# Kernel tuning notes

Measured on AMD Instinct MI355X. Metric: run time of the kernel, lower is better.

## Reference

```python
import jax, jax.numpy as jnp
import numpy as np


def _ln(x, w, b, eps=1e-5):
    m = x.mean(-1, keepdims=True)
    v = jnp.mean((x - m) ** 2, -1, keepdims=True)
    return (x - m) / jnp.sqrt(v + eps) * w + b


def _conv_layer(x, batch, pos, mask, Ncount, wq, bq, wk, bk, wv, bv):
    # x: [N, C] node features; dense-batched to [B, L, C] per to_dense_batch
    B, L = mask.shape
    C = x.shape[-1]
    H = wq.shape[1] // C  # out_channels == hidden == C
    D = C
    xd = jnp.zeros((B, L, C), x.dtype).at[batch, pos].set(x)
    qs = (xd @ wq + bq).reshape(B, L, H, D)
    ks = (xd @ wk + bk).reshape(B, L, H, D)
    vs = (xd @ wv + bv).reshape(B, L, H, D)
    m = mask[:, :, None, None]
    qs = jnp.where(m, qs, 0.0)
    ks = jnp.where(m, ks, 0.0)
    vs = jnp.where(m, vs, 0.0)
    # NOTE: original divides by GLOBAL Frobenius norm of the whole tensor
    qs = qs / jnp.linalg.norm(qs)
    ks = ks / jnp.linalg.norm(ks)
    Nb = Ncount[:, None, None, None]  # [B,1,1,1] node count per graph
    kvs = jnp.einsum('blhm,blhd->bhmd', ks, vs)
    num = jnp.einsum('bnhm,bhmd->bnhd', qs, kvs) + Nb * vs
    ks_sum = ks.sum(1)  # [B,H,D]
    denom = jnp.einsum('bnhm,bhm->bnh', qs, ks_sum)[..., None] + Nb
    out = num / denom  # [B,L,H,D]
    return out[batch, pos].mean(1)  # gather masked rows, mean over heads -> [N, D]


def _forward(x, fc0_w, fc0_b, ln0_w, ln0_b,
             wq0_w, wq0_b, wk0_w, wk0_b, wv0_w, wv0_b, ln1_w, ln1_b,
             wq1_w, wq1_b, wk1_w, wk1_b, wv1_w, wv1_b, ln2_w, ln2_b,
             batch, num_graphs, max_nodes):
    N = x.shape[0]
    B, L = num_graphs, max_nodes
    counts = jax.ops.segment_sum(jnp.ones(N, jnp.int32), batch, num_segments=B)
    starts = jnp.concatenate([jnp.zeros(1, jnp.int32), jnp.cumsum(counts)[:-1]])
    pos = jnp.arange(N) - starts[batch]
    mask = jnp.zeros((B, L), bool).at[batch, pos].set(True)
    Ncount = counts.astype(x.dtype)
    # input projection + LN + ReLU (dropout is identity in eval mode)
    h = jax.nn.relu(_ln(x @ fc0_w + fc0_b, ln0_w, ln0_b))
    prev = h
    h = _conv_layer(h, batch, pos, mask, Ncount, wq0_w, wq0_b, wk0_w, wk0_b, wv0_w, wv0_b)
    h = (h + prev) / 2.0
    h = jax.nn.relu(_ln(h, ln1_w, ln1_b))
    prev = h
    h = _conv_layer(h, batch, pos, mask, Ncount, wq1_w, wq1_b, wk1_w, wk1_b, wv1_w, wv1_b)
    h = (h + prev) / 2.0
    h = jax.nn.relu(_ln(h, ln2_w, ln2_b))
    return h


def setup_inputs() -> dict:
    key = jax.random.key(0)
    ks = jax.random.split(key, 16)
    B, L, Cin, H, D = 16, 2048, 16, 4, 256
    N = B * L
    inp = {}
    inp['x'] = jax.random.normal(ks[0], (N, Cin), jnp.float32)
    inp['batch'] = jnp.repeat(jnp.arange(B), L)  # sorted segment ids, equal graphs
    inp['fc0_w'] = jax.random.normal(ks[1], (Cin, D), jnp.float32) * (1.0 / np.sqrt(Cin))
    inp['fc0_b'] = jnp.zeros((D,), jnp.float32)
    for i in range(3):
        inp[f'ln{i}_w'] = jnp.ones((D,), jnp.float32)
        inp[f'ln{i}_b'] = jnp.zeros((D,), jnp.float32)
    s = 1.0 / np.sqrt(D)
    for i in range(2):
        for j, nm in enumerate(['wq', 'wk', 'wv']):
            inp[f'{nm}{i}_w'] = jax.random.normal(ks[2 + 3 * i + j], (D, H * D), jnp.float32) * s
            inp[f'{nm}{i}_b'] = jnp.zeros((H * D,), jnp.float32)
    inp['num_graphs'] = B
    inp['max_nodes'] = L
    return inp


def reference(x, fc0_w, fc0_b, ln0_w, ln0_b,
              wq0_w, wq0_b, wk0_w, wk0_b, wv0_w, wv0_b, ln1_w, ln1_b,
              wq1_w, wq1_b, wk1_w, wk1_b, wv1_w, wv1_b, ln2_w, ln2_b,
              batch, num_graphs, max_nodes):
    return _forward(x, fc0_w, fc0_b, ln0_w, ln0_b,
                    wq0_w, wq0_b, wk0_w, wk0_b, wv0_w, wv0_b, ln1_w, ln1_b,
                    wq1_w, wq1_b, wk1_w, wk1_b, wv1_w, wv1_b, ln2_w, ln2_b,
                    batch, num_graphs, max_nodes)
```

## Files before the change

kernel.cpp:

```cpp
#include <hip/hip_runtime.h>
#include <stdint.h>


typedef unsigned short u16;
typedef unsigned int u32;
typedef __attribute__((ext_vector_type(8))) short bf16x8;
typedef __attribute__((ext_vector_type(8))) unsigned short u16x8;
typedef __attribute__((ext_vector_type(4))) float f32x4;

#define APAD 264

static __device__ __forceinline__ float bf2f(u16 u) {
  union { u32 i; float f; } c; c.i = ((u32)u) << 16; return c.f;
}
static __device__ __forceinline__ u16 f2bf(float f) {
  union { float ff; u32 i; } c; c.ff = f;
  u32 x = c.i;
  x += 0x7fffu + ((x >> 16) & 1u);
  return (u16)(x >> 16);
}
static __device__ __forceinline__ bf16x8 as_bf(u16x8 v) {
  union { u16x8 a; bf16x8 b; } c; c.a = v; return c.b;
}
static __device__ __forceinline__ float dpp_x1(float v) {
  return __int_as_float(__builtin_amdgcn_mov_dpp(__float_as_int(v), 0xB1, 0xF, 0xF, true));
}
static __device__ __forceinline__ float dpp_x2(float v) {
  return __int_as_float(__builtin_amdgcn_mov_dpp(__float_as_int(v), 0x4E, 0xF, 0xF, true));
}
static __device__ __forceinline__ u32 dpp_x1u(u32 v) {
  return (u32)__builtin_amdgcn_mov_dpp((int)v, 0xB1, 0xF, 0xF, true);
}

__global__ __launch_bounds__(256) void k_prep(
    const float* __restrict__ fc0_w,
    const float* __restrict__ wv0, const float* __restrict__ bv0,
    const float* __restrict__ wv1, const float* __restrict__ bv1,
    u16* __restrict__ w0T,
    u16* __restrict__ w2_0, float* __restrict__ bvm0,
    u16* __restrict__ w2_1, float* __restrict__ bvm1)
{
  const int bid = blockIdx.x, tid = threadIdx.x;
  if (bid < 32) {
    __shared__ u16 t[64][72];
    const int L  = bid >> 4;
    const int ti = (bid >> 2) & 3;
    const int tj = bid & 3;
    const float* wv = L ? wv1 : wv0;
    u16* W2 = L ? w2_1 : w2_0;
    const int cl = tid >> 2, dq = tid & 3;
    #pragma unroll
    for (int e = 0; e < 16; e++) {
      const int dl = dq * 16 + e;
      const float* p = wv + (size_t)(ti * 64 + cl) * 1024 + tj * 64 + dl;
      t[cl][dl] = f2bf(0.25f * (p[0] + p[256] + p[512] + p[768]));
    }
    __syncthreads();
    const int dl = tid >> 2, cq = tid & 3;
    u16x8 v0, v1;
    #pragma unroll
    for (int e = 0; e < 8; e++) { v0[e] = t[cq * 16 + e][dl]; v1[e] = t[cq * 16 + 8 + e][dl]; }
    const int kt = ti * 2 + (cq >> 1);
    const int q0 = (cq & 1) * 2;
    const int d  = tj * 64 + dl;
    u16* dst = W2 + kt * 8192 + d * 32 + q0 * 8;
    *(u16x8*)dst = v0;
    *(u16x8*)(dst + 8) = v1;
  } else {
    const int d = tid;
    u16x8 r0, r1;
    #pragma unroll
    for (int k = 0; k < 8; k++) {
      r0[k] = f2bf(fc0_w[k * 256 + d]);
      r1[k] = f2bf(fc0_w[(k + 8) * 256 + d]);
    }
    *(u16x8*)(w0T + d * 16) = r0;
    *(u16x8*)(w0T + d * 16 + 8) = r1;
    float t0 = 0.f, t1 = 0.f;
    #pragma unroll
    for (int h = 0; h < 4; h++) { t0 += bv0[h * 256 + d]; t1 += bv1[h * 256 + d]; }
    bvm0[d] = 0.25f * t0;
    bvm1[d] = 0.25f * t1;
  }
}

__global__ __launch_bounds__(512, 4) void k_mega(
    const float* __restrict__ x,
    const u16* __restrict__ w0T, const float* __restrict__ fc0_b,
    const float* __restrict__ ln0w, const float* __restrict__ ln0b,
    const u16* __restrict__ w2_0, const float* __restrict__ bvm0,
    const float* __restrict__ ln1w, const float* __restrict__ ln1b,
    const u16* __restrict__ w2_1, const float* __restrict__ bvm1,
    const float* __restrict__ ln2w, const float* __restrict__ ln2b,
    float* __restrict__ out)
{
  __shared__ u16 As[64 * APAD];
  __shared__ u16 Bs[2][8192];
  __shared__ float2 part[64][17];
  __shared__ float stats[64][2];

  const int tid  = threadIdx.x;
  const int lane = tid & 63;
  const int w    = tid >> 6;
  const int wr   = w >> 2;
  const int wc   = w & 3;
  const int fr   = lane & 15;
  const int fq   = lane >> 4;
  const int kc   = fq << 3;
  const int kcB  = (fq ^ ((fr >> 1) & 3)) << 3;
  const int m0   = blockIdx.x * 64;
  const int rbase = wr * 32;
  const int qidx = wc * 4 + (fr >> 2);
  const int swdst = ((tid >> 2) << 5) | (((tid & 3) ^ ((tid >> 3) & 3)) << 3);

  f32x4 acc[2][4];
  #pragma unroll
  for (int i = 0; i < 2; i++)
    #pragma unroll
    for (int j = 0; j < 4; j++)
      acc[i][j] = f32x4{0.f, 0.f, 0.f, 0.f};

  {
    bf16x8 af[2], bg[4];
    if (kc < 16) {
      #pragma unroll
      for (int i = 0; i < 2; i++) {
        const float* xp = x + (size_t)(m0 + rbase + i * 16 + fr) * 16 + kc;
        const f32x4 lo = *(const f32x4*)xp;
        const f32x4 hi = *(const f32x4*)(xp + 4);
        u16x8 v;
        #pragma unroll
        for (int e = 0; e < 4; e++) { v[e] = f2bf(lo[e]); v[4 + e] = f2bf(hi[e]); }
        af[i] = as_bf(v);
      }
      #pragma unroll
      for (int j = 0; j < 4; j++)
        bg[j] = as_bf(*(const u16x8*)(w0T + (wc * 64 + j * 16 + fr) * 16 + kc));
    } else {
      const u16x8 z = {0,0,0,0,0,0,0,0};
      #pragma unroll
      for (int i = 0; i < 2; i++) af[i] = as_bf(z);
      #pragma unroll
      for (int j = 0; j < 4; j++) bg[j] = as_bf(z);
    }
    #pragma unroll
    for (int i = 0; i < 2; i++)
      #pragma unroll
      for (int j = 0; j < 4; j++)
        acc[i][j] = __builtin_amdgcn_mfma_f32_16x16x32_bf16(af[i], bg[j], acc[i][j], 0, 0, 0);
  }

  {
    float vb[4], vw[4], vl[4];
    #pragma unroll
    for (int j = 0; j < 4; j++) {
      const int c = wc * 64 + j * 16 + fr;
      vb[j] = fc0_b[c]; vw[j] = ln0w[c]; vl[j] = ln0b[c];
    }
    #pragma unroll
    for (int i = 0; i < 2; i++)
      #pragma unroll
      for (int r = 0; r < 4; r++) {
        const int row = rbase + i * 16 + fq * 4 + r;
        float s = 0.f, ss = 0.f;
        #pragma unroll
        for (int j = 0; j < 4; j++) {
          const float xv = acc[i][j][r] + vb[j];
          acc[i][j][r] = xv;
          s += xv; ss += xv * xv;
        }
        s += dpp_x1(s);  ss += dpp_x1(ss);
        s += dpp_x2(s);  ss += dpp_x2(ss);
        if ((fr & 3) == 0) part[row][qidx] = float2{s, ss};
      }
    __syncthreads();
    if (tid < 64) {
      float s = 0.f, ss = 0.f;
      #pragma unroll
      for (int k = 0; k < 16; k++) { const float2 v = part[tid][k]; s += v.x; ss += v.y; }
      const float mean = s * (1.0f / 256.0f);
      const float var  = ss * (1.0f / 256.0f) - mean * mean;
      stats[tid][0] = mean;
      stats[tid][1] = rsqrtf(var + 1e-5f);
    }
    __syncthreads();
    #pragma unroll
    for (int i = 0; i < 2; i++)
      #pragma unroll
      for (int r = 0; r < 4; r++) {
        const int row = rbase + i * 16 + fq * 4 + r;
        const float mean = stats[row][0], rstd = stats[row][1];
        #pragma unroll
        for (int j = 0; j < 4; j++) {
          const int col = wc * 64 + j * 16 + fr;
          const float y = fmaxf((acc[i][j][r] - mean) * rstd * vw[j] + vl[j], 0.f);
          const u32 self = f2bf(y);
          const u32 peer = dpp_x1u(self);
          if ((fr & 1) == 0)
            *(u32*)&As[row * APAD + col] = self | (peer << 16);
        }
      }
    __syncthreads();
  }

  #pragma unroll 1
  for (int p = 0; p < 2; p++) {
    const u16* W2 = p ? w2_1 : w2_0;
    const float* bvp = p ? bvm1 : bvm0;
    const float* lw  = p ? ln2w : ln1w;
    const float* lb  = p ? ln2b : ln1b;

    #pragma unroll
    for (int i = 0; i < 2; i++)
      #pragma unroll
      for (int j = 0; j < 4; j++)
        acc[i][j] = f32x4{0.f, 0.f, 0.f, 0.f};

    u16x8 s0 = *(const u16x8*)(W2 + tid * 8);
    u16x8 s1 = *(const u16x8*)(W2 + 4096 + tid * 8);
    *(u16x8*)(&Bs[0][swdst]) = s0;
    *(u16x8*)(&Bs[0][4096 + swdst]) = s1;

    #pragma unroll
    for (int c = 0; c < 8; c++) {
      if (c < 7) {
        s0 = *(const u16x8*)(W2 + (c + 1) * 8192 + tid * 8);
        s1 = *(const u16x8*)(W2 + (c + 1) * 8192 + 4096 + tid * 8);
      }
      __syncthreads();
      const u16* bbase = &Bs[c & 1][0];
      bf16x8 a[2], b[4];
      #pragma unroll
      for (int i = 0; i < 2; i++)
        a[i] = *(const bf16x8*)(As + (rbase + i * 16 + fr) * APAD + c * 32 + kc);
      #pragma unroll
      for (int j = 0; j < 4; j++)
        b[j] = *(const bf16x8*)(bbase + (wc * 64 + j * 16 + fr) * 32 + kcB);
      #pragma unroll
      for (int i = 0; i < 2; i++)
        #pragma unroll
        for (int j = 0; j < 4; j++)
          acc[i][j] = __builtin_amdgcn_mfma_f32_16x16x32_bf16(a[i], b[j], acc[i][j], 0, 0, 0);
      if (c < 7) {
        *(u16x8*)(&Bs[(c + 1) & 1][swdst]) = s0;
        *(u16x8*)(&Bs[(c + 1) & 1][4096 + swdst]) = s1;
      }
    }

    float vb[4], vw[4], vl[4];
    #pragma unroll
    for (int j = 0; j < 4; j++) {
      const int c = wc * 64 + j * 16 + fr;
      vb[j] = bvp[c]; vw[j] = lw[c]; vl[j] = lb[c];
    }
    #pragma unroll
    for (int i = 0; i < 2; i++)
      #pragma unroll
      for (int r = 0; r < 4; r++) {
        const int row = rbase + i * 16 + fq * 4 + r;
        float s = 0.f, ss = 0.f;
        #pragma unroll
        for (int j = 0; j < 4; j++) {
          const int col = wc * 64 + j * 16 + fr;
          const float prev = bf2f(As[row * APAD + col]);
          const float xv = (acc[i][j][r] + vb[j] + prev) * 0.5f;
          acc[i][j][r] = xv;
          s += xv; ss += xv * xv;
        }
        s += dpp_x1(s);  ss += dpp_x1(ss);
        s += dpp_x2(s);  ss += dpp_x2(ss);
        if ((fr & 3) == 0) part[row][qidx] = float2{s, ss};
      }
    __syncthreads();
    if (tid < 64) {
      float s = 0.f, ss = 0.f;
      #pragma unroll
      for (int k = 0; k < 16; k++) { const float2 v = part[tid][k]; s += v.x; ss += v.y; }
      const float mean = s * (1.0f / 256.0f);
      const float var  = ss * (1.0f / 256.0f) - mean * mean;
      stats[tid][0] = mean;
      stats[tid][1] = rsqrtf(var + 1e-5f);
    }
    __syncthreads();
    if (p == 0) {
      #pragma unroll
      for (int i = 0; i < 2; i++)
        #pragma unroll
        for (int r = 0; r < 4; r++) {
          const int row = rbase + i * 16 + fq * 4 + r;
          const float mean = stats[row][0], rstd = stats[row][1];
          #pragma unroll
          for (int j = 0; j < 4; j++) {
            const int col = wc * 64 + j * 16 + fr;
            const float y = fmaxf((acc[i][j][r] - mean) * rstd * vw[j] + vl[j], 0.f);
            const u32 self = f2bf(y);
            const u32 peer = dpp_x1u(self);
            if ((fr & 1) == 0)
              *(u32*)&As[row * APAD + col] = self | (peer << 16);
          }
        }
      __syncthreads();
    } else {
      #pragma unroll
      for (int i = 0; i < 2; i++)
        #pragma unroll
        for (int r = 0; r < 4; r++) {
          const int row = rbase + i * 16 + fq * 4 + r;
          const float mean = stats[row][0], rstd = stats[row][1];
          #pragma unroll
          for (int j = 0; j < 4; j++) {
            const int col = wc * 64 + j * 16 + fr;
            const float y = fmaxf((acc[i][j][r] - mean) * rstd * vw[j] + vl[j], 0.f);
            out[(size_t)(m0 + row) * 256 + col] = y;
          }
        }
    }
  }
}

extern "C" void kernel_launch(void* const* d_in, const int* in_sizes, int n_in,
                              void* d_out, int out_size, void* d_ws, size_t ws_size,
                              hipStream_t stream)
{
  (void)in_sizes; (void)n_in; (void)out_size; (void)ws_size;
  const float* x     = (const float*)d_in[0];
  const float* fc0_w = (const float*)d_in[2];
  const float* fc0_b = (const float*)d_in[3];
  const float* ln0_w = (const float*)d_in[4];
  const float* ln0_b = (const float*)d_in[5];
  const float* ln1_w = (const float*)d_in[6];
  const float* ln1_b = (const float*)d_in[7];
  const float* ln2_w = (const float*)d_in[8];
  const float* ln2_b = (const float*)d_in[9];
  const float* wv0_w = (const float*)d_in[14];
  const float* wv0_b = (const float*)d_in[15];
  const float* wv1_w = (const float*)d_in[20];
  const float* wv1_b = (const float*)d_in[21];

  char* ws = (char*)d_ws;
  u16*   w2_0 = (u16*)(ws);
  u16*   w2_1 = (u16*)(ws + 131072ull);
  u16*   w0T  = (u16*)(ws + 262144ull);
  float* bvm0 = (float*)(ws + 270336ull);
  float* bvm1 = (float*)(ws + 271360ull);

  k_prep<<<33, 256, 0, stream>>>(fc0_w, wv0_w, wv0_b, wv1_w, wv1_b,
                                 w0T, w2_0, bvm0, w2_1, bvm1);
  k_mega<<<512, 512, 0, stream>>>(x, w0T, fc0_b, ln0_w, ln0_b,
                                  w2_0, bvm0, ln1_w, ln1_b,
                                  w2_1, bvm1, ln2_w, ln2_b,
                                  (float*)d_out);
}
```

Measured before the change: 35.31 us.

## Stream weight tiles via direct global-to-LDS loads and keep residual in registers

Weight tiles for the two fused layers now go straight from global memory into LDS with global_load_lds, skipping the staging registers. The first tile of each layer is prefetched early, overlapping the LayerNorm epilogue and the previous layer's last chunk. The swizzle moves to the global-side address. The residual is kept in fp32 registers instead of being re-read from bf16 LDS, bf16 packing uses the hardware v_cvt_pk_bf16_f32 instruction, and a couple of barriers are removed or moved. This costs more registers for the stored residual and relies on careful barrier placement around asynchronous LDS writes.

```diff
diff --git a/kernel.cpp b/kernel.cpp
--- a/kernel.cpp
+++ b/kernel.cpp
@@ -28,8 +28,15 @@
 static __device__ __forceinline__ float dpp_x2(float v) {
   return __int_as_float(__builtin_amdgcn_mov_dpp(__float_as_int(v), 0x4E, 0xF, 0xF, true));
 }
-static __device__ __forceinline__ u32 dpp_x1u(u32 v) {
-  return (u32)__builtin_amdgcn_mov_dpp((int)v, 0xB1, 0xF, 0xF, true);
+static __device__ __forceinline__ u32 pk_bf16(float lo, float hi) {
+  u32 r;
+  asm("v_cvt_pk_bf16_f32 %0, %1, %2" : "=v"(r) : "v"(lo), "v"(hi));
+  return r;
+}
+typedef __attribute__((address_space(1))) const void gv_t;
+typedef __attribute__((address_space(3))) void lv_t;
+static __device__ __forceinline__ void glds16(const u16* g, u16* l) {
+  __builtin_amdgcn_global_load_lds((gv_t*)g, (lv_t*)l, 16, 0, 0);
 }
 
 __global__ __launch_bounds__(256) void k_prep(
@@ -111,9 +118,16 @@
   const int m0   = blockIdx.x * 64;
   const int rbase = wr * 32;
   const int qidx = wc * 4 + (fr >> 2);
-  const int swdst = ((tid >> 2) << 5) | (((tid & 3) ^ ((tid >> 3) & 3)) << 3);
+
+  const int d0 = (w * 2) * 16 + (lane >> 2);
+  const int d1 = (w * 2 + 1) * 16 + (lane >> 2);
+  const int g0 = d0 * 32 + ((lane & 3) ^ ((d0 >> 1) & 3)) * 8;
+  const int g1 = d1 * 32 + ((lane & 3) ^ ((d1 >> 1) & 3)) * 8;
+  const int l0 = (w * 2) * 512;
+  const int l1 = (w * 2 + 1) * 512;
 
   f32x4 acc[2][4];
+  float hprev[2][4][4];
   #pragma unroll
   for (int i = 0; i < 2; i++)
     #pragma unroll
@@ -150,6 +164,9 @@
         acc[i][j] = __builtin_amdgcn_mfma_f32_16x16x32_bf16(af[i], bg[j], acc[i][j], 0, 0, 0);
   }
 
+  glds16(w2_0 + g0, &Bs[0][l0]);
+  glds16(w2_0 + g1, &Bs[0][l1]);
+
   {
     float vb[4], vw[4], vl[4];
     #pragma unroll
@@ -194,13 +211,12 @@
         for (int j = 0; j < 4; j++) {
           const int col = wc * 64 + j * 16 + fr;
           const float y = fmaxf((acc[i][j][r] - mean) * rstd * vw[j] + vl[j], 0.f);
-          const u32 self = f2bf(y);
-          const u32 peer = dpp_x1u(self);
+          hprev[i][j][r] = y;
+          const float yp = dpp_x1(y);
           if ((fr & 1) == 0)
-            *(u32*)&As[row * APAD + col] = self | (peer << 16);
-        }
-      }
-    __syncthreads();
+            *(u32*)&As[row * APAD + col] = pk_bf16(y, yp);
+        }
+      }
   }
 
   #pragma unroll 1
@@ -216,18 +232,17 @@
       for (int j = 0; j < 4; j++)
         acc[i][j] = f32x4{0.f, 0.f, 0.f, 0.f};
 
-    u16x8 s0 = *(const u16x8*)(W2 + tid * 8);
-    u16x8 s1 = *(const u16x8*)(W2 + 4096 + tid * 8);
-    *(u16x8*)(&Bs[0][swdst]) = s0;
-    *(u16x8*)(&Bs[0][4096 + swdst]) = s1;
-
     #pragma unroll
     for (int c = 0; c < 8; c++) {
+      __syncthreads();
       if (c < 7) {
-        s0 = *(const u16x8*)(W2 + (c + 1) * 8192 + tid * 8);
-        s1 = *(const u16x8*)(W2 + (c + 1) * 8192 + 4096 + tid * 8);
-      }
-      __syncthreads();
+        const u16* src = W2 + (c + 1) * 8192;
+        glds16(src + g0, &Bs[(c + 1) & 1][l0]);
+        glds16(src + g1, &Bs[(c + 1) & 1][l1]);
+      } else if (p == 0) {
+        glds16(w2_1 + g0, &Bs[0][l0]);
+        glds16(w2_1 + g1, &Bs[0][l1]);
+      }
       const u16* bbase = &Bs[c & 1][0];
       bf16x8 a[2], b[4];
       #pragma unroll
@@ -241,10 +256,6 @@
         #pragma unroll
         for (int j = 0; j < 4; j++)
           acc[i][j] = __builtin_amdgcn_mfma_f32_16x16x32_bf16(a[i], b[j], acc[i][j], 0, 0, 0);
-      if (c < 7) {
-        *(u16x8*)(&Bs[(c + 1) & 1][swdst]) = s0;
-        *(u16x8*)(&Bs[(c + 1) & 1][4096 + swdst]) = s1;
-      }
     }
 
     float vb[4], vw[4], vl[4];
@@ -261,9 +272,7 @@
         float s = 0.f, ss = 0.f;
         #pragma unroll
         for (int j = 0; j < 4; j++) {
-          const int col = wc * 64 + j * 16 + fr;
-          const float prev = bf2f(As[row * APAD + col]);
-          const float xv = (acc[i][j][r] + vb[j] + prev) * 0.5f;
+          const float xv = (acc[i][j][r] + vb[j] + hprev[i][j][r]) * 0.5f;
           acc[i][j][r] = xv;
           s += xv; ss += xv * xv;
         }
@@ -293,13 +302,12 @@
           for (int j = 0; j < 4; j++) {
             const int col = wc * 64 + j * 16 + fr;
             const float y = fmaxf((acc[i][j][r] - mean) * rstd * vw[j] + vl[j], 0.f);
-            const u32 self = f2bf(y);
-            const u32 peer = dpp_x1u(self);
+            hprev[i][j][r] = y;
+            const float yp = dpp_x1(y);
             if ((fr & 1) == 0)
-              *(u32*)&As[row * APAD + col] = self | (peer << 16);
+              *(u32*)&As[row * APAD + col] = pk_bf16(y, yp);
           }
         }
-      __syncthreads();
     } else {
       #pragma unroll
       for (int i = 0; i < 2; i++)
```

Result: slower. 47.21 us (+33.7%).
